# Kernel optimization log

Hardware: AMD Instinct MI355X
Metric: run time of the kernel (lower is better)

## Reference

```python
import jax, jax.numpy as jnp
import numpy as np

B, S, D, H, L = 2, 2048, 768, 12, 12
DH = D // H
REL_POS_BINS, MAX_REL_POS = 32, 128
REL_2D_POS_BINS, MAX_REL_2D_POS = 64, 256
LN_EPS = 1e-12


def setup_inputs() -> dict:
    key = jax.random.key(0)
    ks = jax.random.split(key, 12)
    s = 0.02
    return {
        "hidden_states": jax.random.normal(ks[0], (B, S, D), jnp.float32),
        "attention_mask": jnp.zeros((B, 1, 1, S), jnp.bool_),  # True = masked
        "position_ids": jnp.sort(jax.random.randint(ks[1], (B, S), 0, 1024), axis=-1),
        "bbox": jax.random.randint(ks[2], (B, S, 4), 0, 1024),
        # stacked per-layer params (torch Linear applied as x @ W + b)
        "q_w": jax.random.normal(ks[3], (L, D, D), jnp.float32) * s,
        "q_b": jnp.zeros((L, D), jnp.float32),
        "k_w": jax.random.normal(ks[4], (L, D, D), jnp.float32) * s,
        "k_b": jnp.zeros((L, D), jnp.float32),
        "v_w": jax.random.normal(ks[5], (L, D, D), jnp.float32) * s,
        "v_b": jnp.zeros((L, D), jnp.float32),
        "o_w": jax.random.normal(ks[6], (L, D, D), jnp.float32) * s,
        "o_b": jnp.zeros((L, D), jnp.float32),
        "ln_g": jnp.ones((L, D), jnp.float32),
        "ln_b": jnp.zeros((L, D), jnp.float32),
        # rel-pos bias heads x buckets (nn.Linear(bins, heads, bias=False).weight)
        "rel_pos_bias_w": jax.random.normal(ks[7], (H, REL_POS_BINS), jnp.float32) * s,
        "rel_x_bias_w": jax.random.normal(ks[8], (H, REL_2D_POS_BINS), jnp.float32) * s,
        "rel_y_bias_w": jax.random.normal(ks[9], (H, REL_2D_POS_BINS), jnp.float32) * s,
    }


def _rel_bucket(rel, num_buckets, max_distance):
    # bidirectional bucketing from Mesh-TF / ErnieLayout
    nb = num_buckets // 2
    ret = (rel > 0).astype(jnp.int32) * nb
    n = jnp.abs(rel).astype(jnp.int32)
    max_exact = nb // 2
    is_small = n < max_exact
    nf = jnp.maximum(n, 1).astype(jnp.float32)  # avoid log(0); masked by is_small
    val_large = max_exact + (
        jnp.log(nf / max_exact) / np.log(max_distance / max_exact) * (nb - max_exact)
    ).astype(jnp.int32)
    val_large = jnp.minimum(val_large, nb - 1)
    return ret + jnp.where(is_small, n, val_large)


def _bias_from_table(ids_1d, table, num_buckets, max_distance):
    # ids_1d: [B,S] int; table: [H, buckets] -> bias [B,H,S,S]
    rel = ids_1d[:, None, :] - ids_1d[:, :, None]  # memory - query
    buckets = _rel_bucket(rel, num_buckets, max_distance)  # [B,S,S]
    return jnp.transpose(table.T[buckets], (0, 3, 1, 2))  # one-hot @ W.T == gather


def _layer_norm(x, g, b):
    m = jnp.mean(x, axis=-1, keepdims=True)
    v = jnp.mean((x - m) ** 2, axis=-1, keepdims=True)
    return (x - m) / jnp.sqrt(v + LN_EPS) * g + b


def reference(hidden_states, attention_mask, position_ids, bbox,
              q_w, q_b, k_w, k_b, v_w, v_b, o_w, o_b, ln_g, ln_b,
              rel_pos_bias_w, rel_x_bias_w, rel_y_bias_w):
    rel_pos = _bias_from_table(position_ids, rel_pos_bias_w, REL_POS_BINS, MAX_REL_POS)
    rel_2d = (_bias_from_table(bbox[:, :, 0], rel_x_bias_w, REL_2D_POS_BINS, MAX_REL_2D_POS)
              + _bias_from_table(bbox[:, :, 3], rel_y_bias_w, REL_2D_POS_BINS, MAX_REL_2D_POS))
    bias = rel_pos + rel_2d  # [B,H,S,S], shared across layers
    neg = jnp.finfo(jnp.float32).min
    inv_sqrt_dh = 1.0 / np.sqrt(DH)

    def layer(h, p):
        qw, qb, kw, kb, vw, vb, ow, ob, g, bb = p
        q = (h @ qw + qb).reshape(B, S, H, DH).transpose(0, 2, 1, 3) * inv_sqrt_dh
        k = (h @ kw + kb).reshape(B, S, H, DH).transpose(0, 2, 1, 3)
        v = (h @ vw + vb).reshape(B, S, H, DH).transpose(0, 2, 1, 3)
        scores = jnp.einsum('bhqd,bhkd->bhqk', q, k) + bias
        scores = jnp.where(attention_mask, neg, scores)
        probs = jax.nn.softmax(scores, axis=-1)
        ctx = jnp.einsum('bhqk,bhkd->bhqd', probs, v).transpose(0, 2, 1, 3).reshape(B, S, D)
        out = ctx @ ow + ob  # ErnieLayoutSelfOutput dense
        return _layer_norm(out + h, g, bb), None

    h, _ = jax.lax.scan(layer, hidden_states,
                        (q_w, q_b, k_w, k_b, v_w, v_b, o_w, o_b, ln_g, ln_b))
    return h
```

## Files before the change

kernel.cpp:

```cpp
#include <hip/hip_runtime.h>


#define BB 2
#define SS 2048
#define DD 768
#define HH 12
#define NLAYER 12
#define MM 4096

typedef unsigned short u16;
typedef unsigned char u8;
typedef __attribute__((ext_vector_type(8))) short bf16x8;
typedef __attribute__((ext_vector_type(4))) float f32x4;
typedef __attribute__((ext_vector_type(2))) float f32x2;

#define LOG2E 1.44269504088896340736f

__device__ __forceinline__ u16 f2bf(float f) {
  unsigned u = __float_as_uint(f);
  unsigned r = (u + 0x7FFFu + ((u >> 16) & 1u)) >> 16;
  return (u16)r;
}
__device__ __forceinline__ unsigned cvtpk(float a, float b) {
  unsigned r;
  asm("v_cvt_pk_bf16_f32 %0, %1, %2" : "=v"(r) : "v"(a), "v"(b));
  return r;
}
__device__ __forceinline__ float exp2v(float x) {
  float r;
  asm("v_exp_f32 %0, %1" : "=v"(r) : "v"(x));
  return r;
}

__device__ __forceinline__ void g2lds16(const void* g, void* l) {
  __builtin_amdgcn_global_load_lds(
      (const __attribute__((address_space(1))) unsigned int*)g,
      (__attribute__((address_space(3))) unsigned int*)l, 16, 0, 0);
}

__global__ __launch_bounds__(256) void k_hb(const float4* __restrict__ x,
                                            uint2* __restrict__ o, int n4) {
  int i = blockIdx.x * 256 + threadIdx.x;
  if (i < n4) {
    float4 v = x[i];
    uint2 r;
    r.x = (unsigned)f2bf(v.x) | ((unsigned)f2bf(v.y) << 16);
    r.y = (unsigned)f2bf(v.z) | ((unsigned)f2bf(v.w) << 16);
    o[i] = r;
  }
}

__device__ __forceinline__ int bucket1(int rel) {
  int ret = rel > 0 ? 16 : 0;
  int n = rel < 0 ? -rel : rel;
  if (n < 8) return ret + n;
  int v = 8 + (int)(logf((float)n * 0.125f) * 2.8853900817779268f);
  return ret + (v < 15 ? v : 15);
}
__device__ __forceinline__ int bucket2(int rel) {
  int ret = rel > 0 ? 32 : 0;
  int n = rel < 0 ? -rel : rel;
  if (n < 16) return ret + n;
  int v = 16 + (int)(logf((float)n * 0.0625f) * 5.7707801635558537f);
  return ret + (v < 31 ? v : 31);
}

__global__ __launch_bounds__(256) void k_bias(
    const int* __restrict__ pos, const int* __restrict__ bbx,
    const unsigned char* __restrict__ msk,
    const float* __restrict__ wp, const float* __restrict__ wx,
    const float* __restrict__ wy, u8* __restrict__ bias) {
  int bid = blockIdx.x;
  int b = bid >> 10, qt = (bid >> 5) & 31, kt = bid & 31;
  __shared__ __align__(16) float swpT[3][32][4], swxT[3][64][4], swyT[3][64][4];
  __shared__ int pq[64], xq[64], yq[64], pk[64], xk[64], yk[64];
  __shared__ unsigned char mk[64];
  int t = threadIdx.x;
  for (int i = t; i < 384; i += 256) {
    int g = i >> 7, idx = i & 127;
    swpT[g][idx >> 2][idx & 3] = wp[(g * 4 + (idx & 3)) * 32 + (idx >> 2)] * LOG2E;
  }
  for (int i = t; i < 768; i += 256) {
    int g = i >> 8, idx = i & 255;
    swxT[g][idx >> 2][idx & 3] = wx[(g * 4 + (idx & 3)) * 64 + (idx >> 2)] * LOG2E;
    swyT[g][idx >> 2][idx & 3] = wy[(g * 4 + (idx & 3)) * 64 + (idx >> 2)] * LOG2E;
  }
  int q0 = qt * 64, k0 = kt * 64;
  if (t < 64) {
    int gi = b * SS + q0 + t;
    pq[t] = pos[gi]; xq[t] = bbx[gi * 4]; yq[t] = bbx[gi * 4 + 3];
  } else if (t < 128) {
    int j = t - 64, gi = b * SS + k0 + j;
    pk[j] = pos[gi]; xk[j] = bbx[gi * 4]; yk[j] = bbx[gi * 4 + 3];
    mk[j] = msk[b * SS + k0 + j];
  }
  __syncthreads();
  int w = t >> 6, l = t & 63;
  int hi = l >> 4;
  int qlr = w * 16 + (l & 15);
  int pql = pq[qlr], xql = xq[qlr], yql = yq[qlr];
  int packed[16];
#pragma unroll
  for (int fn = 0; fn < 4; fn++)
#pragma unroll
    for (int r = 0; r < 4; r++) {
      int kl = fn * 16 + hi * 4 + r;
      int b1 = bucket1(pk[kl] - pql);
      int b2 = bucket2(xk[kl] - xql);
      int b3 = bucket2(yk[kl] - yql);
      packed[fn * 4 + r] = b1 | (b2 << 5) | (b3 << 11) | (mk[kl] ? (1 << 17) : 0);
    }
  for (int hg = 0; hg < 3; hg++) {
    unsigned words[4][4];
#pragma unroll
    for (int j2 = 0; j2 < 8; j2++) {
      float a0[4], a1[4];
      {
        int p = packed[2 * j2];
        f32x4 ap = *(const f32x4*)swpT[hg][p & 31];
        f32x4 bx = *(const f32x4*)swxT[hg][(p >> 5) & 63];
        f32x4 cy = *(const f32x4*)swyT[hg][(p >> 11) & 63];
        bool mm = (p >> 17) != 0;
#pragma unroll
        for (int hh = 0; hh < 4; hh++)
          a0[hh] = mm ? -3.0e38f : (ap[hh] + bx[hh] + cy[hh]);
      }
      {
        int p = packed[2 * j2 + 1];
        f32x4 ap = *(const f32x4*)swpT[hg][p & 31];
        f32x4 bx = *(const f32x4*)swxT[hg][(p >> 5) & 63];
        f32x4 cy = *(const f32x4*)swyT[hg][(p >> 11) & 63];
        bool mm = (p >> 17) != 0;
#pragma unroll
        for (int hh = 0; hh < 4; hh++)
          a1[hh] = mm ? -3.0e38f : (ap[hh] + bx[hh] + cy[hh]);
      }
      int wd = j2 >> 1;
      if ((j2 & 1) == 0) {
#pragma unroll
        for (int hh = 0; hh < 4; hh++)
          words[hh][wd] = __builtin_amdgcn_cvt_pk_fp8_f32(a0[hh], a1[hh], 0, false);
      } else {
#pragma unroll
        for (int hh = 0; hh < 4; hh++)
          words[hh][wd] = __builtin_amdgcn_cvt_pk_fp8_f32(a0[hh], a1[hh],
                                                          words[hh][wd], true);
      }
    }
#pragma unroll
    for (int hh = 0; hh < 4; hh++) {
      int h = hg * 4 + hh;
      u8* dst = bias +
          ((size_t)((b * 12 + h) * 1024 + qt * 32 + kt) * 256 + t) * 16;
      *(uint4*)dst = make_uint4(words[hh][0], words[hh][1], words[hh][2],
                                words[hh][3]);
    }
  }
}

__global__ __launch_bounds__(256) void k_wconv(
    const float* __restrict__ qw, const float* __restrict__ kw,
    const float* __restrict__ vw, const float* __restrict__ ow, int layer,
    u16* __restrict__ wt) {
  int bid = blockIdx.x;
  int g = bid / 144, rr_ = bid % 144, nt = rr_ / 12, kt = rr_ % 12;
  const float* src = g == 0 ? qw : g == 1 ? kw : g == 2 ? vw : ow;
  src += (size_t)layer * DD * DD;
  __shared__ float sm[64][67];
  int t = threadIdx.x, c2 = t & 31, r0 = t >> 5;
#pragma unroll
  for (int p = 0; p < 8; p++) {
    int row = r0 + p * 8;
    float2 v = *(const float2*)&src[(size_t)(kt * 64 + row) * DD + nt * 64 + c2 * 2];
    sm[row][c2 * 2] = v.x;
    sm[row][c2 * 2 + 1] = v.y;
  }
  __syncthreads();
  u16* dst = wt + (size_t)g * DD * DD;
#pragma unroll
  for (int p = 0; p < 8; p++) {
    int n = r0 + p * 8;
    float v0 = sm[c2 * 2][n], v1 = sm[c2 * 2 + 1][n];
    *(unsigned*)&dst[(size_t)(nt * 64 + n) * DD + kt * 64 + c2 * 2] = cvtpk(v0, v1);
  }
}

__device__ __forceinline__ void gemm_core(const u16* __restrict__ A,
                                          const u16* __restrict__ Bt, u16* As,
                                          u16* Bs, f32x4 acc[4][4], int tid) {
  int w = tid >> 6, l = tid & 63;
  int wm = w >> 1, wn = w & 1;
#pragma unroll
  for (int i = 0; i < 4; i++)
#pragma unroll
    for (int j = 0; j < 4; j++) acc[i][j] = f32x4{0.f, 0.f, 0.f, 0.f};
  for (int kt = 0; kt < 12; kt++) {
    __syncthreads();
    int r0 = w * 32;
#pragma unroll
    for (int j = 0; j < 4; j++) {
      int row = r0 + j * 8 + (l >> 3);
      int sl = (l & 7) ^ (row & 7);
      g2lds16(A + (size_t)row * DD + kt * 64 + sl * 8, As + (r0 + j * 8) * 64);
      g2lds16(Bt + (size_t)row * DD + kt * 64 + sl * 8, Bs + (r0 + j * 8) * 64);
    }
    __syncthreads();
#pragma unroll
    for (int kk = 0; kk < 2; kk++) {
      bf16x8 af[4], bfr[4];
#pragma unroll
      for (int fm = 0; fm < 4; fm++) {
        int row = wm * 64 + fm * 16 + (l & 15);
        int slot = (kk * 4 + (l >> 4)) ^ (row & 7);
        af[fm] = *(const bf16x8*)((const char*)As + row * 128 + slot * 16);
      }
#pragma unroll
      for (int fn = 0; fn < 4; fn++) {
        int row = wn * 64 + fn * 16 + (l & 15);
        int slot = (kk * 4 + (l >> 4)) ^ (row & 7);
        bfr[fn] = *(const bf16x8*)((const char*)Bs + row * 128 + slot * 16);
      }
#pragma unroll
      for (int fm = 0; fm < 4; fm++)
#pragma unroll
        for (int fn = 0; fn < 4; fn++)
          acc[fm][fn] = __builtin_amdgcn_mfma_f32_16x16x32_bf16(
              af[fm], bfr[fn], acc[fm][fn], 0, 0, 0);
    }
  }
}

__global__ __launch_bounds__(256) void k_gemm_qkv(
    const u16* __restrict__ hb, const u16* __restrict__ wt,
    const float* __restrict__ qbias, const float* __restrict__ kbias,
    const float* __restrict__ vbias, u16* __restrict__ qo, u16* __restrict__ ko,
    u16* __restrict__ vo) {
  __shared__ __align__(16) u16 As[128 * 64];
  __shared__ __align__(16) u16 Bs[128 * 64];
  int bid = blockIdx.x;
  int mblk = bid / 18, nblk = bid % 18;
  int g = nblk / 6, nb = nblk % 6;
  const u16* A = hb + (size_t)mblk * 128 * DD;
  const u16* Bt = wt + (size_t)g * DD * DD + (size_t)nb * 128 * DD;
  f32x4 acc[4][4];
  gemm_core(A, Bt, As, Bs, acc, threadIdx.x);
  const float* bias = g == 0 ? qbias : g == 1 ? kbias : vbias;
  u16* out = g == 0 ? qo : g == 1 ? ko : vo;
  float scale = g == 0 ? 0.125f * LOG2E : 1.0f;
  int w = threadIdx.x >> 6, l = threadIdx.x & 63;
  int wm = w >> 1, wn = w & 1;
#pragma unroll
  for (int fn = 0; fn < 4; fn++) {
    int col = nb * 128 + wn * 64 + fn * 16 + (l & 15);
    float bval = bias[col];
#pragma unroll
    for (int fm = 0; fm < 4; fm++)
#pragma unroll
      for (int r = 0; r < 4; r++) {
        int row = mblk * 128 + wm * 64 + fm * 16 + ((l >> 4) << 2) + r;
        out[(size_t)row * DD + col] = f2bf((acc[fm][fn][r] + bval) * scale);
      }
  }
}

__global__ __launch_bounds__(256) void k_gemm_o(const u16* __restrict__ ctx,
                                                const u16* __restrict__ wto,
                                                const float* __restrict__ obias,
                                                float* __restrict__ outp) {
  __shared__ __align__(16) u16 As[128 * 64];
  __shared__ __align__(16) u16 Bs[128 * 64];
  int bid = blockIdx.x;
  int mblk = bid / 6, nblk = bid % 6;
  const u16* A = ctx + (size_t)mblk * 128 * DD;
  const u16* Bt = wto + (size_t)nblk * 128 * DD;
  f32x4 acc[4][4];
  gemm_core(A, Bt, As, Bs, acc, threadIdx.x);
  int w = threadIdx.x >> 6, l = threadIdx.x & 63;
  int wm = w >> 1, wn = w & 1;
#pragma unroll
  for (int fn = 0; fn < 4; fn++) {
    int col = nblk * 128 + wn * 64 + fn * 16 + (l & 15);
    float bval = obias[col];
#pragma unroll
    for (int fm = 0; fm < 4; fm++)
#pragma unroll
      for (int r = 0; r < 4; r++) {
        int row = mblk * 128 + wm * 64 + fm * 16 + ((l >> 4) << 2) + r;
        outp[(size_t)row * DD + col] = acc[fm][fn][r] + bval;
      }
  }
}

__global__ __launch_bounds__(256) void k_vt(const u16* __restrict__ vo,
                                            u16* __restrict__ vt) {
  int bid = blockIdx.x;
  int bh = bid >> 5, st = bid & 31;
  int b = bh / 12, h = bh % 12;
  int s0 = st * 64;
  __shared__ u16 sm[64][68];
  int t = threadIdx.x, c = t & 63, r0 = t >> 6;
#pragma unroll
  for (int p = 0; p < 16; p++) {
    int r = r0 + p * 4;
    sm[r][c] = vo[(size_t)(b * SS + s0 + r) * DD + h * 64 + c];
  }
  __syncthreads();
#pragma unroll
  for (int p = 0; p < 16; p++) {
    int d = r0 + p * 4;
    vt[(size_t)(bh * 64 + d) * SS + s0 + c] = sm[c][d];
  }
}

__global__ __launch_bounds__(256) void k_attn(
    const u16* __restrict__ qm, const u16* __restrict__ kmat,
    const u16* __restrict__ vt, const u8* __restrict__ bias,
    u16* __restrict__ ctx) {
  int bid = blockIdx.x;
  int qt = bid & 31, bh = bid >> 5;
  int b = bh / 12, h = bh % 12;
  __shared__ __align__(16) u16 Ks[2][64 * 64];
  __shared__ __align__(16) u16 Vs[2][64 * 64];
  __shared__ __align__(16) u16 Ps[4][16 * 64];
  int tid = threadIdx.x, w = tid >> 6, l = tid & 63;
  int hi = l >> 4, qr = l & 15;
  int q0 = qt * 64;
  const u16* qp = qm + (size_t)(b * SS + q0 + w * 16 + qr) * DD + h * 64 +
                  hi * 8;
  bf16x8 aq0 = *(const bf16x8*)qp;
  bf16x8 aq1 = *(const bf16x8*)(qp + 32);
  const u16* kb_ = kmat + (size_t)(b * SS) * DD + h * 64;
  const u16* vb_ = vt + (size_t)bh * 64 * SS;
  const u8* bb_ = bias + ((size_t)(bh * 32 + qt) * 32 * 256 + tid) * 16;
  f32x4 oa[4];
#pragma unroll
  for (int fn = 0; fn < 4; fn++) oa[fn] = f32x4{0.f, 0.f, 0.f, 0.f};
  f32x4 lacc = f32x4{0.f, 0.f, 0.f, 0.f};
  float m_ = -3.0e38f;
  bf16x8 vones;
#pragma unroll
  for (int i = 0; i < 8; i++) vones[i] = (short)0x3F80;
  int srow = tid >> 3, sc8 = tid & 7;

  auto STAGE = [&](int kt, int buf) {
#pragma unroll
    for (int j = 0; j < 2; j++) {
      int rr = srow + j * 32;
      int sl = sc8 ^ (rr & 7);
      g2lds16(kb_ + (size_t)(kt * 64 + rr) * DD + sl * 8,
              &Ks[buf][tid * 8 + j * 2048]);
      g2lds16(vb_ + (size_t)rr * SS + kt * 64 + sl * 8,
              &Vs[buf][tid * 8 + j * 2048]);
    }
  };

  STAGE(0, 0);
  uint4 bu = *(const uint4*)bb_;
  uint4 nb = bu;
  char* pw = (char*)&Ps[w][0] + qr * 128;
  int qs = (qr & 7) << 4;
  __syncthreads();

  for (int kt = 0; kt < 32; kt++) {
    int buf = kt & 1;
    if (kt < 31) {
      STAGE(kt + 1, buf ^ 1);
      nb = *(const uint4*)(bb_ + (size_t)(kt + 1) * 4096);
    }
    f32x4 sc[4];
    {
      unsigned uw[4] = {bu.x, bu.y, bu.z, bu.w};
#pragma unroll
      for (int fn = 0; fn < 4; fn++) {
        f32x2 p0 = __builtin_amdgcn_cvt_pk_f32_fp8(uw[fn], false);
        f32x2 p1 = __builtin_amdgcn_cvt_pk_f32_fp8(uw[fn], true);
        sc[fn][0] = p0.x; sc[fn][1] = p0.y; sc[fn][2] = p1.x; sc[fn][3] = p1.y;
      }
    }
    __builtin_amdgcn_s_setprio(1);
#pragma unroll
    for (int kk = 0; kk < 2; kk++) {
      bf16x8 aq = kk == 0 ? aq0 : aq1;
#pragma unroll
      for (int fn = 0; fn < 4; fn++) {
        int row = fn * 16 + qr;
        int slot = (kk * 4 + hi) ^ (row & 7);
        bf16x8 bk = *(const bf16x8*)((const char*)&Ks[buf][0] + row * 128 +
                                     slot * 16);
        sc[fn] = __builtin_amdgcn_mfma_f32_16x16x32_bf16(bk, aq, sc[fn],
                                                         0, 0, 0);
      }
    }
    __builtin_amdgcn_s_setprio(0);
    float pm = fmaxf(fmaxf(fmaxf(sc[0][0], sc[0][1]), fmaxf(sc[0][2], sc[0][3])),
                     fmaxf(fmaxf(sc[1][0], sc[1][1]), fmaxf(sc[1][2], sc[1][3])));
    pm = fmaxf(pm,
         fmaxf(fmaxf(fmaxf(sc[2][0], sc[2][1]), fmaxf(sc[2][2], sc[2][3])),
               fmaxf(fmaxf(sc[3][0], sc[3][1]), fmaxf(sc[3][2], sc[3][3]))));
    pm = fmaxf(pm, __shfl_xor(pm, 16));
    pm = fmaxf(pm, __shfl_xor(pm, 32));
    if (__any(pm > m_ + 8.f)) {
      float mn = fmaxf(m_, pm);
      float f = exp2v(m_ - mn);
#pragma unroll
      for (int fn = 0; fn < 4; fn++)
#pragma unroll
        for (int r = 0; r < 4; r++) oa[fn][r] *= f;
#pragma unroll
      for (int r = 0; r < 4; r++) lacc[r] *= f;
      m_ = mn;
    }
#pragma unroll
    for (int fn = 0; fn < 4; fn++)
#pragma unroll
      for (int r = 0; r < 4; r++) sc[fn][r] = exp2v(sc[fn][r] - m_);
#pragma unroll
    for (int fn = 0; fn < 4; fn++) {
      unsigned w0 = cvtpk(sc[fn][0], sc[fn][1]);
      unsigned w1 = cvtpk(sc[fn][2], sc[fn][3]);
      *(uint2*)(pw + ((fn * 32 + hi * 8) ^ qs)) = make_uint2(w0, w1);
    }
    __builtin_amdgcn_s_setprio(1);
#pragma unroll
    for (int ck = 0; ck < 2; ck++) {
      bf16x8 pt = *(const bf16x8*)(pw + ((ck * 64 + hi * 16) ^ qs));
#pragma unroll
      for (int fn = 0; fn < 4; fn++) {
        int row = fn * 16 + qr;
        int slot = (ck * 4 + hi) ^ (row & 7);
        bf16x8 av = *(const bf16x8*)((const char*)&Vs[buf][0] + row * 128 +
                                     slot * 16);
        oa[fn] = __builtin_amdgcn_mfma_f32_16x16x32_bf16(av, pt, oa[fn],
                                                         0, 0, 0);
      }
      lacc = __builtin_amdgcn_mfma_f32_16x16x32_bf16(vones, pt, lacc, 0, 0, 0);
    }
    __builtin_amdgcn_s_setprio(0);
    bu = nb;
    __syncthreads();
  }
  float inv = 1.0f / lacc[0];
  u16* cp = ctx + (size_t)(b * SS + q0 + w * 16 + qr) * DD + h * 64 + hi * 4;
#pragma unroll
  for (int fn = 0; fn < 4; fn++) {
    unsigned w0 = cvtpk(oa[fn][0] * inv, oa[fn][1] * inv);
    unsigned w1 = cvtpk(oa[fn][2] * inv, oa[fn][3] * inv);
    *(uint2*)(cp + fn * 16) = make_uint2(w0, w1);
  }
}

__global__ __launch_bounds__(256) void k_ln(const float* __restrict__ x,
                                            const float* __restrict__ res,
                                            const float* __restrict__ g,
                                            const float* __restrict__ bta,
                                            float* __restrict__ ho,
                                            u16* __restrict__ hbo) {
  int w = threadIdx.x >> 6, l = threadIdx.x & 63;
  int row = blockIdx.x * 4 + w;
  const float* xr = x + (size_t)row * DD;
  const float* rr = res + (size_t)row * DD;
  float v[12];
  float s = 0.f, s2 = 0.f;
#pragma unroll
  for (int j = 0; j < 12; j++) {
    float a = xr[l + j * 64] + rr[l + j * 64];
    v[j] = a;
    s += a;
    s2 += a * a;
  }
#pragma unroll
  for (int m = 1; m < 64; m <<= 1) {
    s += __shfl_xor(s, m);
    s2 += __shfl_xor(s2, m);
  }
  float mean = s * (1.f / 768.f);
  float var = s2 * (1.f / 768.f) - mean * mean;
  float rstd = rsqrtf(var + 1e-12f);
#pragma unroll
  for (int j = 0; j < 12; j++) {
    int c = l + j * 64;
    float y = (v[j] - mean) * rstd * g[c] + bta[c];
    ho[(size_t)row * DD + c] = y;
    hbo[(size_t)row * DD + c] = f2bf(y);
  }
}

extern "C" void kernel_launch(void* const* d_in, const int* in_sizes, int n_in,
                              void* d_out, int out_size, void* d_ws,
                              size_t ws_size, hipStream_t stream) {
  const float* hid = (const float*)d_in[0];
  const unsigned char* msk = (const unsigned char*)d_in[1];
  const int* pos = (const int*)d_in[2];
  const int* bbx = (const int*)d_in[3];
  const float* qw = (const float*)d_in[4];
  const float* qbv = (const float*)d_in[5];
  const float* kw = (const float*)d_in[6];
  const float* kbv = (const float*)d_in[7];
  const float* vw = (const float*)d_in[8];
  const float* vbv = (const float*)d_in[9];
  const float* ow = (const float*)d_in[10];
  const float* obv = (const float*)d_in[11];
  const float* lng = (const float*)d_in[12];
  const float* lnb = (const float*)d_in[13];
  const float* wpb = (const float*)d_in[14];
  const float* wxb = (const float*)d_in[15];
  const float* wyb = (const float*)d_in[16];
  float* outp = (float*)d_out;

  char* p = (char*)d_ws;
  u8* bias = (u8*)p;     p += (size_t)100663296;
  float* hbuf = (float*)p; p += 12582912;
  u16* hb = (u16*)p;     p += 6291456;
  u16* qo = (u16*)p;     p += 6291456;
  u16* ko = (u16*)p;     p += 6291456;
  u16* vo = (u16*)p;     p += 6291456;
  u16* vtb = (u16*)p;    p += 6291456;
  u16* ctxb = (u16*)p;   p += 6291456;
  u16* wtb = (u16*)p;    p += 4718592;
  float* att = (float*)qo;

  k_hb<<<dim3(3072), dim3(256), 0, stream>>>((const float4*)hid, (uint2*)hb,
                                             786432);
  k_bias<<<dim3(2048), dim3(256), 0, stream>>>(pos, bbx, msk, wpb, wxb, wyb,
                                               bias);
  for (int l = 0; l < NLAYER; l++) {
    k_wconv<<<dim3(576), dim3(256), 0, stream>>>(qw, kw, vw, ow, l, wtb);
    k_gemm_qkv<<<dim3(576), dim3(256), 0, stream>>>(
        hb, wtb, qbv + l * DD, kbv + l * DD, vbv + l * DD, qo, ko, vo);
    k_vt<<<dim3(768), dim3(256), 0, stream>>>(vo, vtb);
    k_attn<<<dim3(768), dim3(256), 0, stream>>>(qo, ko, vtb, bias, ctxb);
    k_gemm_o<<<dim3(192), dim3(256), 0, stream>>>(
        ctxb, wtb + (size_t)3 * DD * DD, obv + l * DD, att);
    k_ln<<<dim3(1024), dim3(256), 0, stream>>>(
        att, l == 0 ? hid : (const float*)hbuf, lng + l * DD, lnb + l * DD,
        l == 11 ? outp : hbuf, hb);
  }
}
```

Before: 1.532 ms.

## Split attention over key halves, fuse V transpose into QKV GEMM epilogue

The attention kernel now splits each query tile's key range into two halves, doubling the block count. Each half writes fp32 partial outputs plus a running max and sum, and a new combine kernel merges them with a log-sum-exp rescale. The V projection epilogue writes directly in the transposed layout, which removes the separate transpose kernel and its round trip through memory. The row max now uses v_max3. The costs are extra fp32 partial-output traffic, one more launch per layer, and strided 8-byte stores in the V epilogue.

Result: no change. 1.509 ms (-1.5%).

```diff
diff --git a/kernel.cpp b/kernel.cpp
--- a/kernel.cpp
+++ b/kernel.cpp
@@ -29,6 +29,11 @@
 __device__ __forceinline__ float exp2v(float x) {
   float r;
   asm("v_exp_f32 %0, %1" : "=v"(r) : "v"(x));
+  return r;
+}
+__device__ __forceinline__ float max3f(float a, float b, float c) {
+  float r;
+  asm("v_max3_f32 %0, %1, %2, %3" : "=v"(r) : "v"(a), "v"(b), "v"(c));
   return r;
 }
 
@@ -234,7 +239,7 @@
     const u16* __restrict__ hb, const u16* __restrict__ wt,
     const float* __restrict__ qbias, const float* __restrict__ kbias,
     const float* __restrict__ vbias, u16* __restrict__ qo, u16* __restrict__ ko,
-    u16* __restrict__ vo) {
+    u16* __restrict__ vtb) {
   __shared__ __align__(16) u16 As[128 * 64];
   __shared__ __align__(16) u16 Bs[128 * 64];
   int bid = blockIdx.x;
@@ -244,11 +249,30 @@
   const u16* Bt = wt + (size_t)g * DD * DD + (size_t)nb * 128 * DD;
   f32x4 acc[4][4];
   gemm_core(A, Bt, As, Bs, acc, threadIdx.x);
-  const float* bias = g == 0 ? qbias : g == 1 ? kbias : vbias;
-  u16* out = g == 0 ? qo : g == 1 ? ko : vo;
-  float scale = g == 0 ? 0.125f * LOG2E : 1.0f;
   int w = threadIdx.x >> 6, l = threadIdx.x & 63;
   int wm = w >> 1, wn = w & 1;
+  int hi4 = (l >> 4) << 2;
+  if (g == 2) {
+#pragma unroll
+    for (int fn = 0; fn < 4; fn++) {
+      int col = nb * 128 + wn * 64 + fn * 16 + (l & 15);
+      float bval = vbias[col];
+      int h = col >> 6, d = col & 63;
+#pragma unroll
+      for (int fm = 0; fm < 4; fm++) {
+        int row = mblk * 128 + wm * 64 + fm * 16 + hi4;
+        int bb = row >> 11, s = row & 2047;
+        unsigned p0 = cvtpk(acc[fm][fn][0] + bval, acc[fm][fn][1] + bval);
+        unsigned p1 = cvtpk(acc[fm][fn][2] + bval, acc[fm][fn][3] + bval);
+        *(uint2*)(vtb + ((size_t)(bb * 12 + h) * 64 + d) * 2048 + s) =
+            make_uint2(p0, p1);
+      }
+    }
+    return;
+  }
+  const float* bias = g == 0 ? qbias : kbias;
+  u16* out = g == 0 ? qo : ko;
+  float scale = g == 0 ? 0.125f * LOG2E : 1.0f;
 #pragma unroll
   for (int fn = 0; fn < 4; fn++) {
     int col = nb * 128 + wn * 64 + fn * 16 + (l & 15);
@@ -257,7 +281,7 @@
     for (int fm = 0; fm < 4; fm++)
 #pragma unroll
       for (int r = 0; r < 4; r++) {
-        int row = mblk * 128 + wm * 64 + fm * 16 + ((l >> 4) << 2) + r;
+        int row = mblk * 128 + wm * 64 + fm * 16 + hi4 + r;
         out[(size_t)row * DD + col] = f2bf((acc[fm][fn][r] + bval) * scale);
       }
   }
@@ -291,33 +315,14 @@
   }
 }
 
-__global__ __launch_bounds__(256) void k_vt(const u16* __restrict__ vo,
-                                            u16* __restrict__ vt) {
-  int bid = blockIdx.x;
-  int bh = bid >> 5, st = bid & 31;
-  int b = bh / 12, h = bh % 12;
-  int s0 = st * 64;
-  __shared__ u16 sm[64][68];
-  int t = threadIdx.x, c = t & 63, r0 = t >> 6;
-#pragma unroll
-  for (int p = 0; p < 16; p++) {
-    int r = r0 + p * 4;
-    sm[r][c] = vo[(size_t)(b * SS + s0 + r) * DD + h * 64 + c];
-  }
-  __syncthreads();
-#pragma unroll
-  for (int p = 0; p < 16; p++) {
-    int d = r0 + p * 4;
-    vt[(size_t)(bh * 64 + d) * SS + s0 + c] = sm[c][d];
-  }
-}
-
 __global__ __launch_bounds__(256) void k_attn(
     const u16* __restrict__ qm, const u16* __restrict__ kmat,
     const u16* __restrict__ vt, const u8* __restrict__ bias,
-    u16* __restrict__ ctx) {
+    float* __restrict__ opart, float* __restrict__ mlbuf) {
   int bid = blockIdx.x;
-  int qt = bid & 31, bh = bid >> 5;
+  int split = bid & 1;
+  int rest = bid >> 1;
+  int qt = rest & 31, bh = rest >> 5;
   int b = bh / 12, h = bh % 12;
   __shared__ __align__(16) u16 Ks[2][64 * 64];
   __shared__ __align__(16) u16 Vs[2][64 * 64];
@@ -331,7 +336,8 @@
   bf16x8 aq1 = *(const bf16x8*)(qp + 32);
   const u16* kb_ = kmat + (size_t)(b * SS) * DD + h * 64;
   const u16* vb_ = vt + (size_t)bh * 64 * SS;
-  const u8* bb_ = bias + ((size_t)(bh * 32 + qt) * 32 * 256 + tid) * 16;
+  const u8* bb_ = bias + ((size_t)(bh * 32 + qt) * 32 * 256 + tid) * 16 +
+                  (size_t)split * 16 * 4096;
   f32x4 oa[4];
 #pragma unroll
   for (int fn = 0; fn < 4; fn++) oa[fn] = f32x4{0.f, 0.f, 0.f, 0.f};
@@ -341,6 +347,7 @@
 #pragma unroll
   for (int i = 0; i < 8; i++) vones[i] = (short)0x3F80;
   int srow = tid >> 3, sc8 = tid & 7;
+  int kbase = split * 16;
 
   auto STAGE = [&](int kt, int buf) {
 #pragma unroll
@@ -354,18 +361,18 @@
     }
   };
 
-  STAGE(0, 0);
+  STAGE(kbase, 0);
   uint4 bu = *(const uint4*)bb_;
   uint4 nb = bu;
   char* pw = (char*)&Ps[w][0] + qr * 128;
   int qs = (qr & 7) << 4;
   __syncthreads();
 
-  for (int kt = 0; kt < 32; kt++) {
-    int buf = kt & 1;
-    if (kt < 31) {
-      STAGE(kt + 1, buf ^ 1);
-      nb = *(const uint4*)(bb_ + (size_t)(kt + 1) * 4096);
+  for (int t = 0; t < 16; t++) {
+    int buf = t & 1;
+    if (t < 15) {
+      STAGE(kbase + t + 1, buf ^ 1);
+      nb = *(const uint4*)(bb_ + (size_t)(t + 1) * 4096);
     }
     f32x4 sc[4];
     {
@@ -392,11 +399,14 @@
       }
     }
     __builtin_amdgcn_s_setprio(0);
-    float pm = fmaxf(fmaxf(fmaxf(sc[0][0], sc[0][1]), fmaxf(sc[0][2], sc[0][3])),
-                     fmaxf(fmaxf(sc[1][0], sc[1][1]), fmaxf(sc[1][2], sc[1][3])));
-    pm = fmaxf(pm,
-         fmaxf(fmaxf(fmaxf(sc[2][0], sc[2][1]), fmaxf(sc[2][2], sc[2][3])),
-               fmaxf(fmaxf(sc[3][0], sc[3][1]), fmaxf(sc[3][2], sc[3][3]))));
+    float pa = max3f(sc[0][0], sc[0][1], sc[0][2]);
+    float pb = max3f(sc[0][3], sc[1][0], sc[1][1]);
+    pa = max3f(pa, sc[1][2], sc[1][3]);
+    pb = max3f(pb, sc[2][0], sc[2][1]);
+    pa = max3f(pa, sc[2][2], sc[2][3]);
+    pb = max3f(pb, sc[3][0], sc[3][1]);
+    pa = max3f(pa, sc[3][2], sc[3][3]);
+    float pm = fmaxf(pa, pb);
     pm = fmaxf(pm, __shfl_xor(pm, 16));
     pm = fmaxf(pm, __shfl_xor(pm, 32));
     if (__any(pm > m_ + 8.f)) {
@@ -439,14 +449,40 @@
     bu = nb;
     __syncthreads();
   }
-  float inv = 1.0f / lacc[0];
-  u16* cp = ctx + (size_t)(b * SS + q0 + w * 16 + qr) * DD + h * 64 + hi * 4;
-#pragma unroll
-  for (int fn = 0; fn < 4; fn++) {
-    unsigned w0 = cvtpk(oa[fn][0] * inv, oa[fn][1] * inv);
-    unsigned w1 = cvtpk(oa[fn][2] * inv, oa[fn][3] * inv);
-    *(uint2*)(cp + fn * 16) = make_uint2(w0, w1);
-  }
+  int rit = w * 16 + qr;
+  float* ob = opart + (size_t)bid * 4096 + rit * 64 + hi * 4;
+#pragma unroll
+  for (int fn = 0; fn < 4; fn++)
+    *(f32x4*)(ob + fn * 16) = oa[fn];
+  if (hi == 0) {
+    *(float2*)(mlbuf + ((size_t)bid * 64 + rit) * 2) =
+        make_float2(m_, lacc[0]);
+  }
+}
+
+__global__ __launch_bounds__(256) void k_comb(const float* __restrict__ opart,
+                                              const float* __restrict__ mlbuf,
+                                              u16* __restrict__ ctx) {
+  int t = threadIdx.x;
+  int row = blockIdx.x * 16 + (t >> 4);
+  int dq = (t & 15) * 4;
+  int tid2 = row >> 6, rit = row & 63;
+  int p0i = tid2 * 2, p1i = p0i + 1;
+  float2 ml0 = *(const float2*)(mlbuf + ((size_t)p0i * 64 + rit) * 2);
+  float2 ml1 = *(const float2*)(mlbuf + ((size_t)p1i * 64 + rit) * 2);
+  float m = fmaxf(ml0.x, ml1.x);
+  float w0 = exp2v(ml0.x - m), w1 = exp2v(ml1.x - m);
+  float inv = 1.0f / (ml0.y * w0 + ml1.y * w1);
+  f32x4 o0 = *(const f32x4*)(opart + (size_t)p0i * 4096 + rit * 64 + dq);
+  f32x4 o1 = *(const f32x4*)(opart + (size_t)p1i * 4096 + rit * 64 + dq);
+  int bh = tid2 >> 5, qt = tid2 & 31;
+  int b = bh / 12, h = bh % 12;
+  int q = qt * 64 + rit;
+  unsigned r0 = cvtpk((o0[0] * w0 + o1[0] * w1) * inv,
+                      (o0[1] * w0 + o1[1] * w1) * inv);
+  unsigned r1 = cvtpk((o0[2] * w0 + o1[2] * w1) * inv,
+                      (o0[3] * w0 + o1[3] * w1) * inv);
+  *(uint2*)(ctx + (size_t)(b * SS + q) * DD + h * 64 + dq) = make_uint2(r0, r1);
 }
 
 __global__ __launch_bounds__(256) void k_ln(const float* __restrict__ x,
@@ -513,10 +549,11 @@
   u16* hb = (u16*)p;     p += 6291456;
   u16* qo = (u16*)p;     p += 6291456;
   u16* ko = (u16*)p;     p += 6291456;
-  u16* vo = (u16*)p;     p += 6291456;
   u16* vtb = (u16*)p;    p += 6291456;
   u16* ctxb = (u16*)p;   p += 6291456;
   u16* wtb = (u16*)p;    p += 4718592;
+  float* opart = (float*)p; p += 25165824;
+  float* mlbuf = (float*)p; p += 786432;
   float* att = (float*)qo;
 
   k_hb<<<dim3(3072), dim3(256), 0, stream>>>((const float4*)hid, (uint2*)hb,
@@ -526,9 +563,10 @@
   for (int l = 0; l < NLAYER; l++) {
     k_wconv<<<dim3(576), dim3(256), 0, stream>>>(qw, kw, vw, ow, l, wtb);
     k_gemm_qkv<<<dim3(576), dim3(256), 0, stream>>>(
-        hb, wtb, qbv + l * DD, kbv + l * DD, vbv + l * DD, qo, ko, vo);
-    k_vt<<<dim3(768), dim3(256), 0, stream>>>(vo, vtb);
-    k_attn<<<dim3(768), dim3(256), 0, stream>>>(qo, ko, vtb, bias, ctxb);
+        hb, wtb, qbv + l * DD, kbv + l * DD, vbv + l * DD, qo, ko, vtb);
+    k_attn<<<dim3(1536), dim3(256), 0, stream>>>(qo, ko, vtb, bias, opart,
+                                                 mlbuf);
+    k_comb<<<dim3(3072), dim3(256), 0, stream>>>(opart, mlbuf, ctxb);
     k_gemm_o<<<dim3(192), dim3(256), 0, stream>>>(
         ctxb, wtb + (size_t)3 * DD * DD, obv + l * DD, att);
     k_ln<<<dim3(1024), dim3(256), 0, stream>>>(
```
